# Kernel optimization log

Measured on AMD Instinct MI355X. Metric: run time of the kernel, lower is better.

Reference implementation:

```python
import jax, jax.numpy as jnp
import numpy as np

DELAY = 4
SKIP = 2
NF = 8
HS = 256
EPS = 1e-5


def setup_inputs() -> dict:
    key = jax.random.key(0)
    ks = jax.random.split(key, 11)
    B, NP, NO, T = 16, 512, 512, 2048
    predictor = jax.random.normal(ks[0], (B, NP, T), dtype=jnp.float32)
    to_order = jax.random.normal(ks[1], (B, NO, T), dtype=jnp.float32)
    trilinear = jax.random.normal(ks[2], (NF, NO, NP), dtype=jnp.float32) / np.float32(np.sqrt(NP * NO))
    w_o = jax.random.normal(ks[3], (HS, NO), dtype=jnp.float32) / np.float32(np.sqrt(NO))
    b_o = jax.random.normal(ks[4], (HS,), dtype=jnp.float32) * 0.01
    w_p = jax.random.normal(ks[5], (HS, NP), dtype=jnp.float32) / np.float32(np.sqrt(NP))
    b_p = jax.random.normal(ks[6], (HS,), dtype=jnp.float32) * 0.01
    bn_gamma = jnp.ones((HS,), dtype=jnp.float32)
    bn_beta = jnp.zeros((HS,), dtype=jnp.float32)
    w_out = jax.random.normal(ks[7], (NF, HS), dtype=jnp.float32) / np.float32(np.sqrt(HS))
    b_out = jax.random.normal(ks[8], (NF,), dtype=jnp.float32) * 0.01
    return {"predictor": predictor, "to_order": to_order, "trilinear": trilinear,
            "w_o": w_o, "b_o": b_o, "w_p": w_p, "b_p": b_p,
            "bn_gamma": bn_gamma, "bn_beta": bn_beta, "w_out": w_out, "b_out": b_out}


def reference(predictor, to_order, trilinear, w_o, b_o, w_p, b_p, bn_gamma, bn_beta, w_out, b_out):
    B, NP, T = predictor.shape
    NO = to_order.shape[1]
    tot_latency = DELAY + SKIP * (NF - 1)
    T_r = T - tot_latency
    pred = predictor[:, :, :T_r]          # (B, np, Tr)
    too = to_order[:, :, DELAY:]          # (B, no, T - delay)
    # predictor_product[b,k,t,m] = sum_p pred[b,p,t] * trilinear[k,m,p]
    pp = jnp.einsum('bpt,kmp->bktm', pred, trilinear)           # (B, nf, Tr, no)
    win = jnp.stack([too[:, :, j * SKIP: j * SKIP + T_r] for j in range(NF)], axis=1)  # (B, nf, no, Tr)
    inner = jnp.einsum('bjmt,bktm->bjkt', win, pp)              # (B, nf, nf, Tr)
    # conv1d (kernel 1) heads
    o_proj = jnp.einsum('hm,bmt->bht', w_o, too) + b_o[None, :, None]    # (B, hs, T - delay)
    p_proj = jnp.einsum('hp,bpt->bht', w_p, pred) + b_p[None, :, None]   # (B, hs, Tr)
    o_win = jnp.stack([o_proj[:, :, j * SKIP: j * SKIP + T_r] for j in range(NF)], axis=1)  # (B, nf, hs, Tr)
    h = jax.nn.relu(o_win + p_proj[:, None])                    # (B, nf, hs, Tr)
    # BatchNorm1d (training-mode batch stats) over (B*nf, hs, Tr): stats over axes (0,1,3)
    mean = h.mean(axis=(0, 1, 3), keepdims=True)
    var = h.var(axis=(0, 1, 3), keepdims=True)
    h = (h - mean) * jax.lax.rsqrt(var + EPS) * bn_gamma[None, None, :, None] + bn_beta[None, None, :, None]
    head = jnp.einsum('kh,bjht->bjkt', w_out, h) + b_out[None, None, :, None]
    inner = inner + head
    log_probs = jax.nn.log_softmax(inner, axis=2)               # (B, nf, nf, Tr)
    correct = jnp.einsum('bjjt->bjt', log_probs)                # diagonal j == k
    return correct.mean(axis=2).mean(axis=0)                    # (nf,)
```

## Files before the change

kernel.cpp:

```cpp
#include <hip/hip_runtime.h>
#include <math.h>

constexpr int B_  = 16;
constexpr int NP_ = 512;
constexpr int NO_ = 512;
constexpr int T_  = 2048;
constexpr int NF_ = 8;
constexpr int HS_ = 256;
constexpr int TR_ = 2030;
constexpr int TO_ = 2044;
constexpr int OPLD_ = 2048;
constexpr float EPS_ = 1e-5f;

typedef short bf16x8 __attribute__((ext_vector_type(8)));
typedef float f32x16 __attribute__((ext_vector_type(16)));

__device__ __forceinline__ unsigned short f2bf(float f) {
  union { float f; unsigned int u; } v; v.f = f;
  unsigned int r = v.u + 0x7fffu + ((v.u >> 16) & 1u);
  return (unsigned short)(r >> 16);
}
__device__ __forceinline__ float bf2f(unsigned short u) {
  union { unsigned int u; float f; } v; v.u = ((unsigned int)u) << 16;
  return v.f;
}

typedef const __attribute__((address_space(1))) unsigned int* gas_u32;
typedef __attribute__((address_space(3))) unsigned int* las_u32;
__device__ __forceinline__ void gl16(const void* g, void* l) {
  __builtin_amdgcn_global_load_lds((gas_u32)g, (las_u32)l, 16, 0, 0);
}


__global__ __launch_bounds__(256) void transpose_cvt(
    const float* __restrict__ in, unsigned short* __restrict__ outb) {
  __shared__ float tile[64][65];
  const int c0 = blockIdx.x * 64;
  const int r0 = blockIdx.y * 64;
  const int b  = blockIdx.z;
  const float* ib = in + (size_t)b * 512 * 2048;
  unsigned short* ob = outb + (size_t)b * 2048 * 512;
  for (int i = threadIdx.x; i < 64 * 16; i += 256) {
    const int r = i >> 4, c4 = (i & 15) * 4;
    float4 v = *(const float4*)(ib + (size_t)(r0 + r) * 2048 + c0 + c4);
    tile[r][c4 + 0] = v.x; tile[r][c4 + 1] = v.y;
    tile[r][c4 + 2] = v.z; tile[r][c4 + 3] = v.w;
  }
  __syncthreads();
  for (int i = threadIdx.x; i < 64 * 8; i += 256) {
    const int c = i >> 3, r8 = (i & 7) * 8;
    unsigned int pk[4];
    #pragma unroll
    for (int e = 0; e < 4; ++e)
      pk[e] = (unsigned int)f2bf(tile[r8 + 2 * e][c]) |
              ((unsigned int)f2bf(tile[r8 + 2 * e + 1][c]) << 16);
    *(uint4*)(ob + (size_t)(c0 + c) * 512 + r0 + r8) = *(uint4*)pk;
  }
}

__global__ __launch_bounds__(256) void cvt_bf16(
    const float* __restrict__ in, unsigned short* __restrict__ out, int n) {
  const int i = (blockIdx.x * 256 + threadIdx.x) * 4;
  if (i < n) {
    float4 v = *(const float4*)(in + i);
    ushort4 o; o.x = f2bf(v.x); o.y = f2bf(v.y); o.z = f2bf(v.z); o.w = f2bf(v.w);
    *(ushort4*)(out + i) = o;
  }
}

__global__ __launch_bounds__(256, 2) void proj_mfma(
    const unsigned short* __restrict__ Wbf,
    const unsigned short* __restrict__ Xt,
    const float* __restrict__ bias,
    unsigned short* __restrict__ out,
    int Tlen, int toff) {
  __shared__ char smem[65536];
  char* const Ab[2] = { smem, smem + 16384 };
  char* const Bb[2] = { smem + 32768, smem + 49152 };
  const int tid = threadIdx.x;
  const int l = tid & 63, wv = tid >> 6;
  const int h = l >> 5, tl = l & 31;
  const int mq = wv >> 1, tq = wv & 1;
  const int t0 = blockIdx.x * 128;
  const int m0 = blockIdx.y * 128;
  const int b  = blockIdx.z;
  const unsigned short* Xb = Xt + (size_t)b * T_ * 512;

  int aSrc[4], bSrc[4], ldsO[4];
  #pragma unroll
  for (int i = 0; i < 4; ++i) {
    const int q = (wv << 8) + (i << 6) + l;
    const int r = q >> 3, c8s = (q & 7) ^ (r & 7);
    aSrc[i] = (m0 + r) * 512 + (c8s << 3);
    const int row = min(t0 + toff + r, T_ - 1);
    bSrc[i] = row * 512 + (c8s << 3);
    ldsO[i] = ((wv << 8) + (i << 6)) << 4;
  }

  f32x16 acc[2][2];
  #pragma unroll
  for (int i = 0; i < 2; ++i)
    #pragma unroll
    for (int jj = 0; jj < 2; ++jj)
      #pragma unroll
      for (int e = 0; e < 16; ++e) acc[i][jj][e] = 0.f;

  #pragma unroll
  for (int i = 0; i < 4; ++i) gl16(Wbf + aSrc[i], Ab[0] + ldsO[i]);
  #pragma unroll
  for (int i = 0; i < 4; ++i) gl16(Xb + bSrc[i], Bb[0] + ldsO[i]);
  asm volatile("s_waitcnt vmcnt(0)" ::: "memory");
  __builtin_amdgcn_s_barrier();

  #pragma unroll
  for (int ps = 0; ps < 8; ++ps) {
    const int cb = ps & 1;
    if (ps < 7) {
      const int p0 = (ps + 1) << 6;
      #pragma unroll
      for (int i = 0; i < 4; ++i) gl16(Wbf + p0 + aSrc[i], Ab[cb ^ 1] + ldsO[i]);
      #pragma unroll
      for (int i = 0; i < 4; ++i) gl16(Xb + p0 + bSrc[i], Bb[cb ^ 1] + ldsO[i]);
    }
    const unsigned short* As = (const unsigned short*)Ab[cb];
    const unsigned short* Bs = (const unsigned short*)Bb[cb];
    #pragma unroll
    for (int s = 0; s < 4; ++s) {
      const int k8 = 2 * s + h;
      bf16x8 af[2], bfr[2];
      #pragma unroll
      for (int mt = 0; mt < 2; ++mt) {
        const int rm = 64 * mq + 32 * mt + tl;
        af[mt] = *(const bf16x8*)(As + rm * 64 + ((k8 ^ (rm & 7)) << 3));
      }
      #pragma unroll
      for (int nt = 0; nt < 2; ++nt) {
        const int rt = 64 * tq + 32 * nt + tl;
        bfr[nt] = *(const bf16x8*)(Bs + rt * 64 + ((k8 ^ (rt & 7)) << 3));
      }
      #pragma unroll
      for (int mt = 0; mt < 2; ++mt)
        #pragma unroll
        for (int nt = 0; nt < 2; ++nt)
          acc[mt][nt] = __builtin_amdgcn_mfma_f32_32x32x16_bf16(
              af[mt], bfr[nt], acc[mt][nt], 0, 0, 0);
    }
    asm volatile("s_waitcnt vmcnt(0)" ::: "memory");
    __builtin_amdgcn_s_barrier();
  }
  #pragma unroll
  for (int mt = 0; mt < 2; ++mt)
    #pragma unroll
    for (int nt = 0; nt < 2; ++nt)
      #pragma unroll
      for (int r = 0; r < 16; ++r) {
        const int hs = m0 + 64 * mq + 32 * mt + (r & 3) + 8 * (r >> 2) + 4 * h;
        const int t  = t0 + 64 * tq + 32 * nt + tl;
        if (t < Tlen)
          out[((size_t)b * HS_ + hs) * OPLD_ + t] = f2bf(acc[mt][nt][r] + bias[hs]);
      }
}

__global__ __launch_bounds__(256, 2) void inner_mfma(
    const unsigned short* __restrict__ pred_t,
    const unsigned short* __restrict__ too_t,
    const unsigned short* __restrict__ tri_bf,
    float* __restrict__ inner) {
  __shared__ char smem[77824];
  char* const Pb[2] = { smem, smem + 16384 };
  char* const Tb[2] = { smem + 32768, smem + 49152 };
  char* const TOOM  = smem + 65536;
  char* const TAIL  = smem + 32768;
  const int tid = threadIdx.x;
  const int l = tid & 63, wv = tid >> 6;
  const int h = l >> 5, tl = l & 31;
  const int mh = wv & 1, th = wv >> 1;
  const int t0 = blockIdx.x * 128;
  const int kf0 = blockIdx.y * 2;
  const int b  = blockIdx.z;
  const unsigned short* predB = pred_t + (size_t)b * T_ * NP_;
  const unsigned short* tooB  = too_t  + (size_t)b * T_ * NO_;
  const unsigned short* triK  = tri_bf + (size_t)kf0 * NO_ * NP_;

  int pSrc[4], pLds[4];
  #pragma unroll
  for (int i = 0; i < 4; ++i) {
    const int q = (wv << 8) + (i << 6) + l;
    const int r = q >> 3, c8s = (q & 7) ^ (r & 7);
    pSrc[i] = (t0 + r) * NP_ + (c8s << 3);
    pLds[i] = ((wv << 8) + (i << 6)) << 4;
  }
  int tSrc[4], tLds[4];
  #pragma unroll
  for (int i = 0; i < 4; ++i) {
    const int q = (wv << 8) + (i << 6) + l;
    const int f = q >> 9, qq = q & 511;
    const int r = qq >> 3, c8s = (qq & 7) ^ (r & 7);
    tSrc[i] = f * (NO_ * NP_) + r * NP_ + (c8s << 3);
    tLds[i] = ((wv << 8) + (i << 6)) << 4;
  }
  int oSrc[3], oLds[3];
  #pragma unroll
  for (int i = 0; i < 3; ++i) {
    const int q = wv * 192 + (i << 6) + l;
    const int r = q >> 3, c8s = (q & 7) ^ (r & 7);
    oSrc[i] = (t0 + r) * NO_ + (c8s << 3);
    oLds[i] = (wv * 192 + (i << 6)) << 4;
  }
  int aSrcT[4], aLdsT[4];
  {
    const int ws = (wv >= 2) ? (wv - 2) : 0;
    #pragma unroll
    for (int i = 0; i < 4; ++i) {
      const int q = (ws << 8) + (i << 6) + l;
      const int r = 96 + (q >> 3), c8s = (q & 7) ^ (r & 7);
      aSrcT[i] = min(t0 + r, T_ - 1) * NO_ + (c8s << 3);
      aLdsT[i] = ((ws << 8) + (i << 6)) << 4;
    }
  }

  f32x16 Sacc[2][2];
  #pragma unroll
  for (int f = 0; f < 2; ++f)
    #pragma unroll
    for (int ct = 0; ct < 2; ++ct)
      #pragma unroll
      for (int e = 0; e < 16; ++e) Sacc[f][ct][e] = 0.f;

  for (int mc = 0; mc < 8; ++mc) {
    const int m0 = mc << 6;
    const int mOff = m0 * NP_;
    __builtin_amdgcn_s_barrier();
    #pragma unroll
    for (int i = 0; i < 3; ++i) gl16(tooB + m0 + oSrc[i], TOOM + oLds[i]);
    #pragma unroll
    for (int i = 0; i < 4; ++i) gl16(triK + mOff + tSrc[i], Tb[0] + tLds[i]);
    #pragma unroll
    for (int i = 0; i < 4; ++i) gl16(predB + pSrc[i], Pb[0] + pLds[i]);
    asm volatile("s_waitcnt vmcnt(0)" ::: "memory");
    __builtin_amdgcn_s_barrier();

    f32x16 Qacc[2][2];
    #pragma unroll
    for (int f = 0; f < 2; ++f)
      #pragma unroll
      for (int nt = 0; nt < 2; ++nt)
        #pragma unroll
        for (int e = 0; e < 16; ++e) Qacc[f][nt][e] = 0.f;

    #pragma unroll
    for (int ps = 0; ps < 8; ++ps) {
      const int cb = ps & 1;
      if (ps < 7) {
        const int p1 = (ps + 1) << 6;
        #pragma unroll
        for (int i = 0; i < 4; ++i)
          gl16(triK + mOff + p1 + tSrc[i], Tb[cb ^ 1] + tLds[i]);
        #pragma unroll
        for (int i = 0; i < 4; ++i)
          gl16(predB + p1 + pSrc[i], Pb[cb ^ 1] + pLds[i]);
      }
      const unsigned short* predS = (const unsigned short*)Pb[cb];
      const unsigned short* triS  = (const unsigned short*)Tb[cb];
      #pragma unroll
      for (int s = 0; s < 4; ++s) {
        const int k8 = 2 * s + h;
        const int swz = (k8 ^ (tl & 7)) << 3;
        bf16x8 a[2], bp[2];
        #pragma unroll
        for (int f = 0; f < 2; ++f)
          a[f] = *(const bf16x8*)(triS + f * 4096 + ((mh << 5) + tl) * 64 + swz);
        #pragma unroll
        for (int nt = 0; nt < 2; ++nt)
          bp[nt] = *(const bf16x8*)(predS + ((th << 6) + (nt << 5) + tl) * 64 + swz);
        #pragma unroll
        for (int f = 0; f < 2; ++f)
          #pragma unroll
          for (int nt = 0; nt < 2; ++nt)
            Qacc[f][nt] = __builtin_amdgcn_mfma_f32_32x32x16_bf16(
                a[f], bp[nt], Qacc[f][nt], 0, 0, 0);
      }
      if (ps == 7 && wv >= 2) {
        #pragma unroll
        for (int i = 0; i < 4; ++i)
          gl16(tooB + m0 + aSrcT[i], TAIL + aLdsT[i]);
      }
      asm volatile("s_waitcnt vmcnt(0)" ::: "memory");
      __builtin_amdgcn_s_barrier();
    }
    #pragma unroll
    for (int f = 0; f < 2; ++f)
      #pragma unroll
      for (int nt = 0; nt < 2; ++nt) {
        unsigned short* QSw = (unsigned short*)(Pb[f] + (((th << 1) + nt) << 12));
        #pragma unroll
        for (int rp = 0; rp < 8; ++rp) {
          const int r = rp << 1;
          const int m = (mh << 5) + (r & 3) + ((r >> 2) << 3) + (h << 2);
          const int c8 = m >> 3, ml = m & 7;
          const int rX = (tl & 24) | ((tl ^ c8) & 7);
          const unsigned int pk = (unsigned int)f2bf(Qacc[f][nt][r]) |
                                  ((unsigned int)f2bf(Qacc[f][nt][r + 1]) << 16);
          *(unsigned int*)(QSw + (((c8 << 5) + rX) << 3) + ml) = pk;
        }
      }
    asm volatile("s_waitcnt lgkmcnt(0)" ::: "memory");
    __builtin_amdgcn_s_barrier();
    #pragma unroll
    for (int s = 0; s < 4; ++s) {
      const int k8 = 2 * s + h;
      bf16x8 atoo[2];
      #pragma unroll
      for (int ct = 0; ct < 2; ++ct) {
        const int rbase = (wv + ct) << 5;
        const int rr = rbase + tl;
        const unsigned short* tb = (rbase < 96)
            ? (const unsigned short*)TOOM + (size_t)rr * 64
            : (const unsigned short*)TAIL + (size_t)(rr - 96) * 64;
        atoo[ct] = *(const bf16x8*)(tb + ((k8 ^ (rr & 7)) << 3));
      }
      const int rqX = (tl & 24) | ((tl ^ k8) & 7);
      #pragma unroll
      for (int f = 0; f < 2; ++f) {
        const bf16x8 bq = *(const bf16x8*)((const unsigned short*)(Pb[f] + (wv << 12)) +
                                           (((k8 << 5) + rqX) << 3));
        #pragma unroll
        for (int ct = 0; ct < 2; ++ct)
          Sacc[f][ct] = __builtin_amdgcn_mfma_f32_32x32x16_bf16(atoo[ct], bq, Sacc[f][ct], 0, 0, 0);
      }
    }
  }
  __syncthreads();
  const int tglob = t0 + (wv << 5) + tl;
  float* SW = (float*)smem + (wv << 11);
  #pragma unroll
  for (int f = 0; f < 2; ++f) {
    #pragma unroll
    for (int ct = 0; ct < 2; ++ct)
      #pragma unroll
      for (int r = 0; r < 16; ++r) {
        const int cc = (ct << 5) + (r & 3) + ((r >> 2) << 3) + (h << 2);
        SW[(cc << 5) + tl] = Sacc[f][ct][r];
      }
    if (tglob < TR_) {
      #pragma unroll
      for (int jj = 0; jj < 4; ++jj) {
        const int j = (jj << 1) + h;
        const float v = SW[((tl + 4 + 2 * j) << 5) + tl];
        inner[(((size_t)b * NF_ + j) * NF_ + (kf0 + f)) * TR_ + tglob] = v;
      }
    }
  }
}

__global__ __launch_bounds__(256) void bn_stats(
    const unsigned short* __restrict__ op, const unsigned short* __restrict__ pp,
    float* __restrict__ partials) {
  const int hh = blockIdx.x, b = blockIdx.y;
  const unsigned short* oprow = op + ((size_t)b * HS_ + hh) * OPLD_;
  const unsigned short* pprow = pp + ((size_t)b * HS_ + hh) * OPLD_;
  float s = 0.f, s2 = 0.f;
  for (int t = threadIdx.x; t < TR_; t += 256) {
    const float pv = bf2f(pprow[t]);
    #pragma unroll
    for (int j = 0; j < NF_; ++j) {
      float r = bf2f(oprow[t + 2 * j]) + pv;
      r = fmaxf(r, 0.f);
      s += r; s2 += r * r;
    }
  }
  __shared__ float red[256], red2[256];
  red[threadIdx.x] = s; red2[threadIdx.x] = s2;
  __syncthreads();
  for (int st = 128; st > 0; st >>= 1) {
    if (threadIdx.x < st) {
      red[threadIdx.x]  += red[threadIdx.x + st];
      red2[threadIdx.x] += red2[threadIdx.x + st];
    }
    __syncthreads();
  }
  if (threadIdx.x == 0) {
    partials[b * HS_ + hh]            = red[0];
    partials[B_ * HS_ + b * HS_ + hh] = red2[0];
  }
}

__global__ __launch_bounds__(256) void bn_finalize(
    const float* __restrict__ partials, const float* __restrict__ gamma,
    const float* __restrict__ beta, const float* __restrict__ w_out,
    const float* __restrict__ b_out, float* __restrict__ w_eff,
    float* __restrict__ cvec) {
  const int hh = threadIdx.x;
  float s = 0.f, s2 = 0.f;
  for (int b = 0; b < B_; ++b) {
    s  += partials[b * HS_ + hh];
    s2 += partials[B_ * HS_ + b * HS_ + hh];
  }
  const float cnt  = (float)B_ * NF_ * TR_;
  const float mean = s / cnt;
  const float var  = s2 / cnt - mean * mean;
  const float scale = gamma[hh] * rsqrtf(var + EPS_);
  const float shift = beta[hh] - mean * scale;
  #pragma unroll
  for (int k = 0; k < NF_; ++k) w_eff[k * HS_ + hh] = w_out[k * HS_ + hh] * scale;
  __shared__ float red[256];
  for (int k = 0; k < NF_; ++k) {
    red[hh] = w_out[k * HS_ + hh] * shift;
    __syncthreads();
    for (int st = 128; st > 0; st >>= 1) {
      if (hh < st) red[hh] += red[hh + st];
      __syncthreads();
    }
    if (hh == 0) cvec[k] = b_out[k] + red[0];
    __syncthreads();
  }
}

__global__ __launch_bounds__(256) void head_final(
    const unsigned short* __restrict__ op, const unsigned short* __restrict__ pp,
    const float* __restrict__ w_eff, const float* __restrict__ cvec,
    const float* __restrict__ inner, float* __restrict__ part3) {
  __shared__ float opS[288 * 20];
  __shared__ float ppS[256 * 20];
  __shared__ float weS[8][256];
  __shared__ float red[4][5];
  const int tid = threadIdx.x;
  const int t0 = blockIdx.x * 256;
  const int b  = blockIdx.y;
  const int jh = blockIdx.z;
  for (int i = tid; i < 8 * 256; i += 256) weS[i >> 8][i & 255] = w_eff[i];
  float acc[4][8] = {};
  const unsigned short* opb = op + (size_t)b * HS_ * OPLD_;
  const unsigned short* ppb = pp + (size_t)b * HS_ * OPLD_;
  for (int hc = 0; hc < 16; ++hc) {
    const int h0 = hc << 4;
    __syncthreads();
    for (int idx = tid; idx < 576; idx += 256) {
      const int r = idx / 36, cc = (idx - r * 36) << 3;
      const int g = min(t0 + cc, OPLD_ - 8);
      uint4 v = *(const uint4*)(opb + (size_t)(h0 + r) * OPLD_ + g);
      #pragma unroll
      for (int e = 0; e < 4; ++e) {
        const unsigned int u = (&v.x)[e];
        opS[(cc + 2 * e) * 20 + r]     = bf2f((unsigned short)(u & 0xffffu));
        opS[(cc + 2 * e + 1) * 20 + r] = bf2f((unsigned short)(u >> 16));
      }
    }
    for (int idx = tid; idx < 512; idx += 256) {
      const int r = idx >> 5, cc = (idx & 31) << 3;
      uint4 v = *(const uint4*)(ppb + (size_t)(h0 + r) * OPLD_ + t0 + cc);
      #pragma unroll
      for (int e = 0; e < 4; ++e) {
        const unsigned int u = (&v.x)[e];
        ppS[(cc + 2 * e) * 20 + r]     = bf2f((unsigned short)(u & 0xffffu));
        ppS[(cc + 2 * e + 1) * 20 + r] = bf2f((unsigned short)(u >> 16));
      }
    }
    __syncthreads();
    float pv[16];
    #pragma unroll
    for (int i = 0; i < 4; ++i) {
      float4 q = *(const float4*)(ppS + tid * 20 + 4 * i);
      pv[4 * i + 0] = q.x; pv[4 * i + 1] = q.y;
      pv[4 * i + 2] = q.z; pv[4 * i + 3] = q.w;
    }
    #pragma unroll
    for (int jj = 0; jj < 4; ++jj) {
      const int col = tid + 2 * ((jh << 2) + jj);
      #pragma unroll
      for (int i = 0; i < 4; ++i) {
        float4 ov = *(const float4*)(opS + col * 20 + 4 * i);
        #pragma unroll
        for (int e = 0; e < 4; ++e) {
          const float r = fmaxf((&ov.x)[e] + pv[4 * i + e], 0.f);
          #pragma unroll
          for (int k = 0; k < 8; ++k) acc[jj][k] += weS[k][h0 + 4 * i + e] * r;
        }
      }
    }
  }
  const int t = t0 + tid;
  float sj[4];
  #pragma unroll
  for (int jj = 0; jj < 4; ++jj) {
    if (t < TR_) {
      const int j = (jh << 2) + jj;
      float v[8]; float mx = -1e30f;
      #pragma unroll
      for (int k = 0; k < 8; ++k) {
        v[k] = acc[jj][k] + cvec[k] +
               inner[(((size_t)b * NF_ + j) * NF_ + k) * TR_ + t];
        mx = fmaxf(mx, v[k]);
      }
      float se = 0.f;
      #pragma unroll
      for (int k = 0; k < 8; ++k) se += expf(v[k] - mx);
      sj[jj] = v[j] - mx - logf(se);
    } else sj[jj] = 0.f;
  }
  #pragma unroll
  for (int jj = 0; jj < 4; ++jj)
    #pragma unroll
    for (int off = 32; off > 0; off >>= 1) sj[jj] += __shfl_down(sj[jj], off);
  if ((tid & 63) == 0) {
    const int wv = tid >> 6;
    #pragma unroll
    for (int jj = 0; jj < 4; ++jj) red[jj][wv] = sj[jj];
  }
  __syncthreads();
  if (tid < 4) {
    const float s = red[tid][0] + red[tid][1] + red[tid][2] + red[tid][3];
    const int j = (jh << 2) + tid;
    part3[(j * B_ + b) * 8 + blockIdx.x] = s;
  }
}

__global__ void final_out(const float* __restrict__ part3, float* __restrict__ out) {
  const int j = threadIdx.x;
  if (j < NF_) {
    float s = 0.f;
    for (int i = 0; i < B_ * 8; ++i) s += part3[j * B_ * 8 + i];
    out[j] = s / ((float)B_ * (float)TR_);
  }
}

extern "C" void kernel_launch(void* const* d_in, const int* in_sizes, int n_in,
                              void* d_out, int out_size, void* d_ws, size_t ws_size,
                              hipStream_t stream) {
  const float* predictor = (const float*)d_in[0];
  const float* to_order  = (const float*)d_in[1];
  const float* trilinear = (const float*)d_in[2];
  const float* w_o   = (const float*)d_in[3];
  const float* b_o   = (const float*)d_in[4];
  const float* w_p   = (const float*)d_in[5];
  const float* b_p   = (const float*)d_in[6];
  const float* bn_g  = (const float*)d_in[7];
  const float* bn_b  = (const float*)d_in[8];
  const float* w_out = (const float*)d_in[9];
  const float* b_out = (const float*)d_in[10];
  float* out = (float*)d_out;

  char* w = (char*)d_ws;
  unsigned short* pred_t = (unsigned short*)w; w += (size_t)B_ * T_ * NP_ * 2;
  unsigned short* too_t  = (unsigned short*)w; w += (size_t)B_ * T_ * NO_ * 2;
  unsigned short* tri_bf = (unsigned short*)w; w += (size_t)NF_ * NO_ * NP_ * 2;
  unsigned short* wo_bf  = (unsigned short*)w; w += (size_t)HS_ * NO_ * 2;
  unsigned short* wp_bf  = (unsigned short*)w; w += (size_t)HS_ * NP_ * 2;
  unsigned short* o_proj = (unsigned short*)w; w += (size_t)B_ * HS_ * OPLD_ * 2;
  unsigned short* p_proj = (unsigned short*)w; w += (size_t)B_ * HS_ * OPLD_ * 2;
  float* inner    = (float*)w; w += (size_t)B_ * NF_ * NF_ * TR_ * 4;
  float* partials = (float*)w; w += (size_t)2 * B_ * HS_ * 4;
  float* w_eff    = (float*)w; w += (size_t)NF_ * HS_ * 4;
  float* cvec     = (float*)w; w += 256;
  float* part3    = (float*)w; w += (size_t)NF_ * B_ * 8 * 4;

  transpose_cvt<<<dim3(32, 8, 16), 256, 0, stream>>>(predictor, pred_t);
  transpose_cvt<<<dim3(32, 8, 16), 256, 0, stream>>>(to_order, too_t);
  cvt_bf16<<<2048, 256, 0, stream>>>(trilinear, tri_bf, NF_ * NO_ * NP_);
  cvt_bf16<<<128, 256, 0, stream>>>(w_o, wo_bf, HS_ * NO_);
  cvt_bf16<<<128, 256, 0, stream>>>(w_p, wp_bf, HS_ * NP_);

  proj_mfma<<<dim3(16, 2, 16), 256, 0, stream>>>(wo_bf, too_t, b_o, o_proj, TO_, 4);
  proj_mfma<<<dim3(16, 2, 16), 256, 0, stream>>>(wp_bf, pred_t, b_p, p_proj, TR_, 0);

  inner_mfma<<<dim3(16, 4, 16), 256, 0, stream>>>(pred_t, too_t, tri_bf, inner);

  bn_stats<<<dim3(HS_, B_), 256, 0, stream>>>(o_proj, p_proj, partials);
  bn_finalize<<<1, 256, 0, stream>>>(partials, bn_g, bn_b, w_out, b_out, w_eff, cvec);
  head_final<<<dim3(8, B_, 2), 256, 0, stream>>>(o_proj, p_proj, w_eff, cvec, inner, part3);
  final_out<<<1, 64, 0, stream>>>(part3, out);
}
```

Before: 375.6 us.

## Vectorize bn_stats loads, split head_final across more blocks, raise MFMA wave priority

The change bundles three unrelated tweaks. bn_stats now has each thread load 8 consecutive bf16 values with 128-bit loads and reuse them across the 8 shifted windows, instead of doing scalar strided loads. head_final halves its time tile to 128 and splits the j dimension across two thread halves, doubling the grid to 256 blocks so the GPU has more parallelism; part3 and final_out are resized to match. In inner_mfma, s_setprio wraps the MFMA loop so waves doing matrix math get issue priority over waves issuing loads.

```diff
diff --git a/kernel.cpp b/kernel.cpp
--- a/kernel.cpp
+++ b/kernel.cpp
@@ -262,6 +262,7 @@
       }
       const unsigned short* predS = (const unsigned short*)Pb[cb];
       const unsigned short* triS  = (const unsigned short*)Tb[cb];
+      __builtin_amdgcn_s_setprio(1);
       #pragma unroll
       for (int s = 0; s < 4; ++s) {
         const int k8 = 2 * s + h;
@@ -280,6 +281,7 @@
             Qacc[f][nt] = __builtin_amdgcn_mfma_f32_32x32x16_bf16(
                 a[f], bp[nt], Qacc[f][nt], 0, 0, 0);
       }
+      __builtin_amdgcn_s_setprio(0);
       if (ps == 7 && wv >= 2) {
         #pragma unroll
         for (int i = 0; i < 4; ++i)
@@ -360,13 +362,37 @@
   const unsigned short* oprow = op + ((size_t)b * HS_ + hh) * OPLD_;
   const unsigned short* pprow = pp + ((size_t)b * HS_ + hh) * OPLD_;
   float s = 0.f, s2 = 0.f;
-  for (int t = threadIdx.x; t < TR_; t += 256) {
-    const float pv = bf2f(pprow[t]);
-    #pragma unroll
-    for (int j = 0; j < NF_; ++j) {
-      float r = bf2f(oprow[t + 2 * j]) + pv;
-      r = fmaxf(r, 0.f);
-      s += r; s2 += r * r;
+  const int t8 = threadIdx.x * 8;
+  if (t8 < TR_) {
+    uint4 pv4 = *(const uint4*)(pprow + t8);
+    uint4 ov[3];
+    ov[0] = *(const uint4*)(oprow + t8);
+    ov[1] = *(const uint4*)(oprow + t8 + 8);
+    ov[2] = *(const uint4*)(oprow + t8 + 16);
+    float ppf[8], opf[24];
+    #pragma unroll
+    for (int i = 0; i < 4; ++i) {
+      const unsigned int u = (&pv4.x)[i];
+      ppf[2 * i]     = bf2f((unsigned short)(u & 0xffffu));
+      ppf[2 * i + 1] = bf2f((unsigned short)(u >> 16));
+    }
+    #pragma unroll
+    for (int g = 0; g < 3; ++g)
+      #pragma unroll
+      for (int i = 0; i < 4; ++i) {
+        const unsigned int u = (&ov[g].x)[i];
+        opf[8 * g + 2 * i]     = bf2f((unsigned short)(u & 0xffffu));
+        opf[8 * g + 2 * i + 1] = bf2f((unsigned short)(u >> 16));
+      }
+    #pragma unroll
+    for (int e = 0; e < 8; ++e) {
+      if (t8 + e < TR_) {
+        #pragma unroll
+        for (int j = 0; j < NF_; ++j) {
+          float r = fmaxf(opf[e + 2 * j] + ppf[e], 0.f);
+          s += r; s2 += r * r;
+        }
+      }
     }
   }
   __shared__ float red[256], red2[256];
@@ -420,23 +446,24 @@
     const unsigned short* __restrict__ op, const unsigned short* __restrict__ pp,
     const float* __restrict__ w_eff, const float* __restrict__ cvec,
     const float* __restrict__ inner, float* __restrict__ part3) {
-  __shared__ float opS[288 * 20];
-  __shared__ float ppS[256 * 20];
+  __shared__ float opS[144 * 20];
+  __shared__ float ppS[128 * 20];
   __shared__ float weS[8][256];
-  __shared__ float red[4][5];
+  __shared__ float red[4][2];
   const int tid = threadIdx.x;
-  const int t0 = blockIdx.x * 256;
+  const int tl = tid & 127, jp = tid >> 7;
+  const int t0 = blockIdx.x * 128;
   const int b  = blockIdx.y;
   const int jh = blockIdx.z;
   for (int i = tid; i < 8 * 256; i += 256) weS[i >> 8][i & 255] = w_eff[i];
-  float acc[4][8] = {};
+  float acc[2][8] = {};
   const unsigned short* opb = op + (size_t)b * HS_ * OPLD_;
   const unsigned short* ppb = pp + (size_t)b * HS_ * OPLD_;
   for (int hc = 0; hc < 16; ++hc) {
     const int h0 = hc << 4;
     __syncthreads();
-    for (int idx = tid; idx < 576; idx += 256) {
-      const int r = idx / 36, cc = (idx - r * 36) << 3;
+    for (int idx = tid; idx < 288; idx += 256) {
+      const int r = idx / 18, cc = (idx - r * 18) << 3;
       const int g = min(t0 + cc, OPLD_ - 8);
       uint4 v = *(const uint4*)(opb + (size_t)(h0 + r) * OPLD_ + g);
       #pragma unroll
@@ -446,8 +473,8 @@
         opS[(cc + 2 * e + 1) * 20 + r] = bf2f((unsigned short)(u >> 16));
       }
     }
-    for (int idx = tid; idx < 512; idx += 256) {
-      const int r = idx >> 5, cc = (idx & 31) << 3;
+    {
+      const int r = tid >> 4, cc = (tid & 15) << 3;
       uint4 v = *(const uint4*)(ppb + (size_t)(h0 + r) * OPLD_ + t0 + cc);
       #pragma unroll
       for (int e = 0; e < 4; ++e) {
@@ -460,13 +487,13 @@
     float pv[16];
     #pragma unroll
     for (int i = 0; i < 4; ++i) {
-      float4 q = *(const float4*)(ppS + tid * 20 + 4 * i);
+      float4 q = *(const float4*)(ppS + tl * 20 + 4 * i);
       pv[4 * i + 0] = q.x; pv[4 * i + 1] = q.y;
       pv[4 * i + 2] = q.z; pv[4 * i + 3] = q.w;
     }
     #pragma unroll
-    for (int jj = 0; jj < 4; ++jj) {
-      const int col = tid + 2 * ((jh << 2) + jj);
+    for (int jj = 0; jj < 2; ++jj) {
+      const int col = tl + 2 * ((jh << 2) + (jp << 1) + jj);
       #pragma unroll
       for (int i = 0; i < 4; ++i) {
         float4 ov = *(const float4*)(opS + col * 20 + 4 * i);
@@ -479,12 +506,12 @@
       }
     }
   }
-  const int t = t0 + tid;
-  float sj[4];
-  #pragma unroll
-  for (int jj = 0; jj < 4; ++jj) {
+  const int t = t0 + tl;
+  float sj[2];
+  #pragma unroll
+  for (int jj = 0; jj < 2; ++jj) {
     if (t < TR_) {
-      const int j = (jh << 2) + jj;
+      const int j = (jh << 2) + (jp << 1) + jj;
       float v[8]; float mx = -1e30f;
       #pragma unroll
       for (int k = 0; k < 8; ++k) {
@@ -499,19 +526,20 @@
     } else sj[jj] = 0.f;
   }
   #pragma unroll
-  for (int jj = 0; jj < 4; ++jj)
+  for (int jj = 0; jj < 2; ++jj)
     #pragma unroll
     for (int off = 32; off > 0; off >>= 1) sj[jj] += __shfl_down(sj[jj], off);
   if ((tid & 63) == 0) {
     const int wv = tid >> 6;
     #pragma unroll
-    for (int jj = 0; jj < 4; ++jj) red[jj][wv] = sj[jj];
+    for (int jj = 0; jj < 2; ++jj) red[wv][jj] = sj[jj];
   }
   __syncthreads();
   if (tid < 4) {
-    const float s = red[tid][0] + red[tid][1] + red[tid][2] + red[tid][3];
-    const int j = (jh << 2) + tid;
-    part3[(j * B_ + b) * 8 + blockIdx.x] = s;
+    const int qp = tid >> 1, qj = tid & 1;
+    const float s = red[2 * qp][qj] + red[2 * qp + 1][qj];
+    const int j = (jh << 2) + (qp << 1) + qj;
+    part3[(j * B_ + b) * 16 + blockIdx.x] = s;
   }
 }
 
@@ -519,7 +547,7 @@
   const int j = threadIdx.x;
   if (j < NF_) {
     float s = 0.f;
-    for (int i = 0; i < B_ * 8; ++i) s += part3[j * B_ * 8 + i];
+    for (int i = 0; i < B_ * 16; ++i) s += part3[j * B_ * 16 + i];
     out[j] = s / ((float)B_ * (float)TR_);
   }
 }
@@ -552,7 +580,7 @@
   float* partials = (float*)w; w += (size_t)2 * B_ * HS_ * 4;
   float* w_eff    = (float*)w; w += (size_t)NF_ * HS_ * 4;
   float* cvec     = (float*)w; w += 256;
-  float* part3    = (float*)w; w += (size_t)NF_ * B_ * 8 * 4;
+  float* part3    = (float*)w; w += (size_t)NF_ * B_ * 16 * 4;
 
   transpose_cvt<<<dim3(32, 8, 16), 256, 0, stream>>>(predictor, pred_t);
   transpose_cvt<<<dim3(32, 8, 16), 256, 0, stream>>>(to_order, too_t);
@@ -567,6 +595,6 @@
 
   bn_stats<<<dim3(HS_, B_), 256, 0, stream>>>(o_proj, p_proj, partials);
   bn_finalize<<<1, 256, 0, stream>>>(partials, bn_g, bn_b, w_out, b_out, w_eff, cvec);
-  head_final<<<dim3(8, B_, 2), 256, 0, stream>>>(o_proj, p_proj, w_eff, cvec, inner, part3);
+  head_final<<<dim3(16, B_, 2), 256, 0, stream>>>(o_proj, p_proj, w_eff, cvec, inner, part3);
   final_out<<<1, 64, 0, stream>>>(part3, out);
 }
```

Result: faster. 349.5 us (-6.9%).
